# Optimization experiments

Measured on AMD Instinct MI355X. Metric: run time of the kernel, lower is better.

The kernel has to match this reference:

```python
import jax, jax.numpy as jnp
import numpy as np


def setup_inputs() -> dict:
    key = jax.random.key(0)
    B, T, C = 8, 4096, 768
    k1, k2, k3, k4 = jax.random.split(key, 4)
    # Per-channel time-decay (w) and time-first (u) weights; real RWKV uses
    # negative decay but the log-domain max-subtraction math is stable either way.
    w = jax.random.normal(k1, (C,), dtype=jnp.float32)
    u = jax.random.normal(k2, (C,), dtype=jnp.float32)
    k = jax.random.normal(k3, (B, T, C), dtype=jnp.float32)
    v = jax.random.normal(k4, (B, T, C), dtype=jnp.float32)
    return {"B": B, "T": T, "C": C, "w": w, "u": u, "k": k, "v": v}


def reference(B, T, C, w, u, k, v):
    # Faithful JAX port of wkv_pytorch: numerically-stable log-domain RWKV
    # WKV recurrence, vectorized over (B, C) and scanned over T.
    NEG_INF = -1e38
    wf = w.astype(jnp.float32)
    uf = u.astype(jnp.float32)
    kf = k.astype(jnp.float32)
    vf = v.astype(jnp.float32)

    def step(carry, inp):
        aa, bb, pp = carry           # each (B, C)
        kt, vt = inp                 # each (B, C)
        ww = uf + kt                 # u broadcast over batch
        p = jnp.maximum(pp, ww)
        e1 = jnp.exp(pp - p)
        e2 = jnp.exp(ww - p)
        yt = (e1 * aa + e2 * vt) / (e1 * bb + e2)
        ww2 = wf + pp
        p2 = jnp.maximum(ww2, kt)
        e1b = jnp.exp(ww2 - p2)
        e2b = jnp.exp(kt - p2)
        return (e1b * aa + e2b * vt, e1b * bb + e2b, p2), yt

    Bn, Cn = kf.shape[0], kf.shape[2]
    init = (
        jnp.zeros((Bn, Cn), jnp.float32),
        jnp.zeros((Bn, Cn), jnp.float32),
        jnp.full((Bn, Cn), NEG_INF, jnp.float32),
    )
    kT = jnp.swapaxes(kf, 0, 1)  # (T, B, C) for scan over time
    vT = jnp.swapaxes(vf, 0, 1)
    _, y = jax.lax.scan(step, init, (kT, vT))
    y = jnp.swapaxes(y, 0, 1)    # back to (B, T, C)
    return y.astype(k.dtype)
```

## Files before the change

### kernel.cpp

```cpp
#include <hip/hip_runtime.h>
#include <math.h>


#define NEG_INF (-1e38f)

__global__ void wkv_chunk_state(const float* __restrict__ w,
                                const float* __restrict__ k,
                                const float* __restrict__ v,
                                float* __restrict__ sa,
                                float* __restrict__ sb,
                                float* __restrict__ sp,
                                int B, int T, int C, int L, int NC) {
    int tid = blockIdx.x * blockDim.x + threadIdx.x;
    int BC = B * C;
    if (tid >= BC * NC) return;
    int j  = tid / BC;
    int bc = tid - j * BC;
    int b  = bc / C;
    int c  = bc - b * C;

    float wc = w[c];
    const float* kp = k + ((size_t)b * T + (size_t)j * L) * C + c;
    const float* vp = v + ((size_t)b * T + (size_t)j * L) * C + c;

    float aa = 0.f, bb = 0.f, pp = NEG_INF;
    #pragma unroll 4
    for (int t = 0; t < L; ++t) {
        float kt = *kp; kp += C;
        float vt = *vp; vp += C;
        float ww = wc + pp;
        float p  = fmaxf(ww, kt);
        float e1 = __expf(ww - p);
        float e2 = __expf(kt - p);
        aa = e1 * aa + e2 * vt;
        bb = e1 * bb + e2;
        pp = p;
    }
    sa[tid] = aa;
    sb[tid] = bb;
    sp[tid] = pp;
}

__global__ void wkv_prefix(const float* __restrict__ w,
                           float* __restrict__ sa,
                           float* __restrict__ sb,
                           float* __restrict__ sp,
                           int B, int C, int L, int NC) {
    int bc = blockIdx.x * blockDim.x + threadIdx.x;
    int BC = B * C;
    if (bc >= BC) return;
    int c = bc % C;
    float wL = w[c] * (float)L;

    float aa = 0.f, bb = 0.f, pp = NEG_INF;
    for (int j = 0; j < NC; ++j) {
        int idx = j * BC + bc;
        float la = sa[idx];
        float lb = sb[idx];
        float lp = sp[idx];
        sa[idx] = aa;
        sb[idx] = bb;
        sp[idx] = pp;
        float ppd = pp + wL;
        float p   = fmaxf(ppd, lp);
        float e1  = __expf(ppd - p);
        float e2  = __expf(lp - p);
        aa = e1 * aa + e2 * la;
        bb = e1 * bb + e2 * lb;
        pp = p;
    }
}

__global__ void wkv_out(const float* __restrict__ w,
                        const float* __restrict__ u,
                        const float* __restrict__ k,
                        const float* __restrict__ v,
                        const float* __restrict__ sa,
                        const float* __restrict__ sb,
                        const float* __restrict__ sp,
                        float* __restrict__ y,
                        int B, int T, int C, int L, int NC) {
    int tid = blockIdx.x * blockDim.x + threadIdx.x;
    int BC = B * C;
    if (tid >= BC * NC) return;
    int j  = tid / BC;
    int bc = tid - j * BC;
    int b  = bc / C;
    int c  = bc - b * C;

    float wc = w[c];
    float uc = u[c];
    size_t base = ((size_t)b * T + (size_t)j * L) * C + c;
    const float* kp = k + base;
    const float* vp = v + base;
    float*       yp = y + base;

    float aa = sa[tid], bb = sb[tid], pp = sp[tid];

    #pragma unroll 4
    for (int t = 0; t < L; ++t) {
        float kt = *kp; kp += C;
        float vt = *vp; vp += C;
        float ww = uc + kt;
        float p  = fmaxf(pp, ww);
        float e1 = __expf(pp - p);
        float e2 = __expf(ww - p);
        float num = e1 * aa + e2 * vt;
        float den = e1 * bb + e2;
        *yp = __fdividef(num, den); yp += C;
        float ww2 = wc + pp;
        float p2  = fmaxf(ww2, kt);
        float e1b = __expf(ww2 - p2);
        float e2b = __expf(kt - p2);
        aa = e1b * aa + e2b * vt;
        bb = e1b * bb + e2b;
        pp = p2;
    }
}

extern "C" void kernel_launch(void* const* d_in, const int* in_sizes, int n_in,
                              void* d_out, int out_size, void* d_ws, size_t ws_size,
                              hipStream_t stream) {
    const float* w = (const float*)d_in[3];
    const float* u = (const float*)d_in[4];
    const float* k = (const float*)d_in[5];
    const float* v = (const float*)d_in[6];
    float* y = (float*)d_out;

    const int C  = in_sizes[3];
    const int BT = in_sizes[5] / C;
    const int T  = 4096;
    const int B  = BT / T;

    int NC = 64;
    while (NC > 1 && ((size_t)3 * B * C * NC * sizeof(float) > ws_size || (T % NC) != 0))
        NC >>= 1;
    const int L = T / NC;

    const int BC    = B * C;
    const int total = BC * NC;
    float* sa = (float*)d_ws;
    float* sb = sa + total;
    float* sp = sb + total;

    const int blk = 256;
    wkv_chunk_state<<<(total + blk - 1) / blk, blk, 0, stream>>>(w, k, v, sa, sb, sp, B, T, C, L, NC);
    wkv_prefix<<<(BC + blk - 1) / blk, blk, 0, stream>>>(w, sa, sb, sp, B, C, L, NC);
    wkv_out<<<(total + blk - 1) / blk, blk, 0, stream>>>(w, u, k, v, sa, sb, sp, y, B, T, C, L, NC);
}
```

Measured before the change: 105.2 us.

## Vectorize WKV chunk kernels with float2, register prefetch, single-exp steps, more chunks

Gives each block one (batch, chunk) pair, with each thread owning two adjacent channels loaded as float2. Next-group k/v values are prefetched into registers while the current group is computed. Each recurrence step now uses one exp of -|d| and a select instead of two exps. The chunk count doubles to 128, and launch bounds of 384 threads are set. The aim is better memory-level parallelism and fewer transcendental ops. The cost is a hard dependence on C being even and equal to twice the block size, and more register pressure.

```diff
diff --git a/kernel.cpp b/kernel.cpp
--- a/kernel.cpp
+++ b/kernel.cpp
@@ -3,42 +3,81 @@
 
 
 #define NEG_INF (-1e38f)
-
-__global__ void wkv_chunk_state(const float* __restrict__ w,
-                                const float* __restrict__ k,
-                                const float* __restrict__ v,
-                                float* __restrict__ sa,
-                                float* __restrict__ sb,
-                                float* __restrict__ sp,
-                                int B, int T, int C, int L, int NC) {
-    int tid = blockIdx.x * blockDim.x + threadIdx.x;
-    int BC = B * C;
-    if (tid >= BC * NC) return;
-    int j  = tid / BC;
-    int bc = tid - j * BC;
-    int b  = bc / C;
-    int c  = bc - b * C;
-
-    float wc = w[c];
-    const float* kp = k + ((size_t)b * T + (size_t)j * L) * C + c;
-    const float* vp = v + ((size_t)b * T + (size_t)j * L) * C + c;
-
-    float aa = 0.f, bb = 0.f, pp = NEG_INF;
-    #pragma unroll 4
-    for (int t = 0; t < L; ++t) {
-        float kt = *kp; kp += C;
-        float vt = *vp; vp += C;
-        float ww = wc + pp;
-        float p  = fmaxf(ww, kt);
-        float e1 = __expf(ww - p);
-        float e2 = __expf(kt - p);
-        aa = e1 * aa + e2 * vt;
-        bb = e1 * bb + e2;
-        pp = p;
-    }
-    sa[tid] = aa;
-    sb[tid] = bb;
-    sp[tid] = pp;
+#define GSZ 4
+
+__device__ __forceinline__ void wkv_step(float& aa, float& bb, float& pp,
+                                         float wc, float kt, float vt) {
+    float ww = wc + pp;
+    float p  = fmaxf(ww, kt);
+    float d  = ww - kt;
+    float e  = __expf(-fabsf(d));
+    float e1 = (d >= 0.f) ? 1.f : e;
+    float e2 = (d >= 0.f) ? e   : 1.f;
+    aa = e1 * aa + e2 * vt;
+    bb = e1 * bb + e2;
+    pp = p;
+}
+
+__device__ __forceinline__ float wkv_ostep(float aa, float bb, float pp,
+                                           float uc, float kt, float vt) {
+    float ww = uc + kt;
+    float d  = pp - ww;
+    float e  = __expf(-fabsf(d));
+    float e1 = (d >= 0.f) ? 1.f : e;
+    float e2 = (d >= 0.f) ? e   : 1.f;
+    return __fdividef(e1 * aa + e2 * vt, e1 * bb + e2);
+}
+
+__global__ __launch_bounds__(384, 6)
+void wkv_chunk_state(const float* __restrict__ w,
+                     const float* __restrict__ kg,
+                     const float* __restrict__ vg,
+                     float* __restrict__ sa,
+                     float* __restrict__ sb,
+                     float* __restrict__ sp,
+                     int B, int T, int C, int L, int NC) {
+    const int bj  = blockIdx.x;
+    const int b   = bj / NC;
+    const int j   = bj - b * NC;
+    const int tid = threadIdx.x;
+    const int C2  = C >> 1;
+
+    const float2* kp = (const float2*)(kg + ((size_t)b * T + (size_t)j * L) * C) + tid;
+    const float2* vp = (const float2*)(vg + ((size_t)b * T + (size_t)j * L) * C) + tid;
+    const float2  wc = ((const float2*)w)[tid];
+
+    float aa0 = 0.f, bb0 = 0.f, pp0 = NEG_INF;
+    float aa1 = 0.f, bb1 = 0.f, pp1 = NEG_INF;
+
+    float2 kb[GSZ], vb[GSZ];
+    #pragma unroll
+    for (int g = 0; g < GSZ; ++g) { kb[g] = kp[g * C2]; vb[g] = vp[g * C2]; }
+
+    for (int t0 = 0; t0 < L - GSZ; t0 += GSZ) {
+        float2 kn[GSZ], vn[GSZ];
+        #pragma unroll
+        for (int g = 0; g < GSZ; ++g) {
+            kn[g] = kp[(t0 + GSZ + g) * C2];
+            vn[g] = vp[(t0 + GSZ + g) * C2];
+        }
+        #pragma unroll
+        for (int g = 0; g < GSZ; ++g) {
+            wkv_step(aa0, bb0, pp0, wc.x, kb[g].x, vb[g].x);
+            wkv_step(aa1, bb1, pp1, wc.y, kb[g].y, vb[g].y);
+        }
+        #pragma unroll
+        for (int g = 0; g < GSZ; ++g) { kb[g] = kn[g]; vb[g] = vn[g]; }
+    }
+    #pragma unroll
+    for (int g = 0; g < GSZ; ++g) {
+        wkv_step(aa0, bb0, pp0, wc.x, kb[g].x, vb[g].x);
+        wkv_step(aa1, bb1, pp1, wc.y, kb[g].y, vb[g].y);
+    }
+
+    const int base = j * (B * C) + b * C + 2 * tid;
+    *(float2*)(sa + base) = make_float2(aa0, aa1);
+    *(float2*)(sb + base) = make_float2(bb0, bb1);
+    *(float2*)(sp + base) = make_float2(pp0, pp1);
 }
 
 __global__ void wkv_prefix(const float* __restrict__ w,
@@ -58,9 +97,7 @@
         float la = sa[idx];
         float lb = sb[idx];
         float lp = sp[idx];
-        sa[idx] = aa;
-        sb[idx] = bb;
-        sp[idx] = pp;
+        sa[idx] = aa; sb[idx] = bb; sp[idx] = pp;
         float ppd = pp + wL;
         float p   = fmaxf(ppd, lp);
         float e1  = __expf(ppd - p);
@@ -71,50 +108,68 @@
     }
 }
 
-__global__ void wkv_out(const float* __restrict__ w,
-                        const float* __restrict__ u,
-                        const float* __restrict__ k,
-                        const float* __restrict__ v,
-                        const float* __restrict__ sa,
-                        const float* __restrict__ sb,
-                        const float* __restrict__ sp,
-                        float* __restrict__ y,
-                        int B, int T, int C, int L, int NC) {
-    int tid = blockIdx.x * blockDim.x + threadIdx.x;
-    int BC = B * C;
-    if (tid >= BC * NC) return;
-    int j  = tid / BC;
-    int bc = tid - j * BC;
-    int b  = bc / C;
-    int c  = bc - b * C;
-
-    float wc = w[c];
-    float uc = u[c];
-    size_t base = ((size_t)b * T + (size_t)j * L) * C + c;
-    const float* kp = k + base;
-    const float* vp = v + base;
-    float*       yp = y + base;
-
-    float aa = sa[tid], bb = sb[tid], pp = sp[tid];
-
-    #pragma unroll 4
-    for (int t = 0; t < L; ++t) {
-        float kt = *kp; kp += C;
-        float vt = *vp; vp += C;
-        float ww = uc + kt;
-        float p  = fmaxf(pp, ww);
-        float e1 = __expf(pp - p);
-        float e2 = __expf(ww - p);
-        float num = e1 * aa + e2 * vt;
-        float den = e1 * bb + e2;
-        *yp = __fdividef(num, den); yp += C;
-        float ww2 = wc + pp;
-        float p2  = fmaxf(ww2, kt);
-        float e1b = __expf(ww2 - p2);
-        float e2b = __expf(kt - p2);
-        aa = e1b * aa + e2b * vt;
-        bb = e1b * bb + e2b;
-        pp = p2;
+__global__ __launch_bounds__(384, 6)
+void wkv_out(const float* __restrict__ w,
+             const float* __restrict__ u,
+             const float* __restrict__ kg,
+             const float* __restrict__ vg,
+             const float* __restrict__ sa,
+             const float* __restrict__ sb,
+             const float* __restrict__ sp,
+             float* __restrict__ y,
+             int B, int T, int C, int L, int NC) {
+    const int bj  = blockIdx.x;
+    const int b   = bj / NC;
+    const int j   = bj - b * NC;
+    const int tid = threadIdx.x;
+    const int C2  = C >> 1;
+
+    const size_t rowbase = ((size_t)b * T + (size_t)j * L) * C;
+    const float2* kp = (const float2*)(kg + rowbase) + tid;
+    const float2* vp = (const float2*)(vg + rowbase) + tid;
+    float2*       yp = (float2*)(y + rowbase) + tid;
+    const float2  wc = ((const float2*)w)[tid];
+    const float2  uc = ((const float2*)u)[tid];
+
+    const int base = j * (B * C) + b * C + 2 * tid;
+    float2 a2 = *(const float2*)(sa + base);
+    float2 b2 = *(const float2*)(sb + base);
+    float2 p2 = *(const float2*)(sp + base);
+    float aa0 = a2.x, bb0 = b2.x, pp0 = p2.x;
+    float aa1 = a2.y, bb1 = b2.y, pp1 = p2.y;
+
+    float2 kb[GSZ], vb[GSZ];
+    #pragma unroll
+    for (int g = 0; g < GSZ; ++g) { kb[g] = kp[g * C2]; vb[g] = vp[g * C2]; }
+
+    for (int t0 = 0; t0 < L - GSZ; t0 += GSZ) {
+        float2 kn[GSZ], vn[GSZ];
+        #pragma unroll
+        for (int g = 0; g < GSZ; ++g) {
+            kn[g] = kp[(t0 + GSZ + g) * C2];
+            vn[g] = vp[(t0 + GSZ + g) * C2];
+        }
+        #pragma unroll
+        for (int g = 0; g < GSZ; ++g) {
+            float2 yo;
+            yo.x = wkv_ostep(aa0, bb0, pp0, uc.x, kb[g].x, vb[g].x);
+            yo.y = wkv_ostep(aa1, bb1, pp1, uc.y, kb[g].y, vb[g].y);
+            yp[(t0 + g) * C2] = yo;
+            wkv_step(aa0, bb0, pp0, wc.x, kb[g].x, vb[g].x);
+            wkv_step(aa1, bb1, pp1, wc.y, kb[g].y, vb[g].y);
+        }
+        #pragma unroll
+        for (int g = 0; g < GSZ; ++g) { kb[g] = kn[g]; vb[g] = vn[g]; }
+    }
+    const int tl = L - GSZ;
+    #pragma unroll
+    for (int g = 0; g < GSZ; ++g) {
+        float2 yo;
+        yo.x = wkv_ostep(aa0, bb0, pp0, uc.x, kb[g].x, vb[g].x);
+        yo.y = wkv_ostep(aa1, bb1, pp1, uc.y, kb[g].y, vb[g].y);
+        yp[(tl + g) * C2] = yo;
+        wkv_step(aa0, bb0, pp0, wc.x, kb[g].x, vb[g].x);
+        wkv_step(aa1, bb1, pp1, wc.y, kb[g].y, vb[g].y);
     }
 }
 
@@ -132,8 +187,9 @@
     const int T  = 4096;
     const int B  = BT / T;
 
-    int NC = 64;
-    while (NC > 1 && ((size_t)3 * B * C * NC * sizeof(float) > ws_size || (T % NC) != 0))
+    int NC = 128;
+    while (NC > 1 && ((size_t)3 * B * C * NC * sizeof(float) > ws_size ||
+                      (T % NC) != 0 || ((T / NC) % GSZ) != 0))
         NC >>= 1;
     const int L = T / NC;
 
@@ -143,8 +199,10 @@
     float* sb = sa + total;
     float* sp = sb + total;
 
-    const int blk = 256;
-    wkv_chunk_state<<<(total + blk - 1) / blk, blk, 0, stream>>>(w, k, v, sa, sb, sp, B, T, C, L, NC);
-    wkv_prefix<<<(BC + blk - 1) / blk, blk, 0, stream>>>(w, sa, sb, sp, B, C, L, NC);
-    wkv_out<<<(total + blk - 1) / blk, blk, 0, stream>>>(w, u, k, v, sa, sb, sp, y, B, T, C, L, NC);
-}
+    const int nblk = B * NC;
+    const int bthr = C / 2;
+
+    wkv_chunk_state<<<nblk, bthr, 0, stream>>>(w, k, v, sa, sb, sp, B, T, C, L, NC);
+    wkv_prefix<<<(BC + 255) / 256, 256, 0, stream>>>(w, sa, sb, sp, B, C, L, NC);
+    wkv_out<<<nblk, bthr, 0, stream>>>(w, u, k, v, sa, sb, sp, y, B, T, C, L, NC);
+}
```

After: 125.2 us. 1.19x slower.
